# Optimization experiments

Hardware: AMD Instinct MI355X
Metric: run time of the kernel (lower is better)

Reference implementation:

```python
import jax, jax.numpy as jnp
import numpy as np

B, S, T = 128, 2048, 128


def setup_inputs() -> dict:
    key = jax.random.key(0)
    k1, k2, k3, k4, k5, k6 = jax.random.split(key, 6)
    logit = jax.random.normal(k1, (B, S, T), jnp.float32)
    target = jax.random.randint(k2, (B, S), 0, T, dtype=jnp.int32)
    seq_lens = jax.random.randint(k3, (B,), 1, S + 1, dtype=jnp.int32)
    transitions = 0.1 * jax.random.normal(k4, (T, T), jnp.float32)
    start_transitions = 0.1 * jax.random.normal(k5, (T,), jnp.float32)
    end_transitions = 0.1 * jax.random.normal(k6, (T,), jnp.float32)
    return dict(logit=logit, target=target, seq_lens=seq_lens,
                transitions=transitions, start_transitions=start_transitions,
                end_transitions=end_transitions)


def reference(logit, target, seq_lens, transitions, start_transitions, end_transitions):
    # logit: [B,S,T] batch-first; CRF works time-first like the torch code's transpose(0,1)
    em = jnp.transpose(logit, (1, 0, 2))          # [S,B,T]
    tg = target.T                                  # [S,B]
    mask = jnp.arange(S)[:, None] < seq_lens[None, :]  # [S,B]

    # ---- loss: -mean log-likelihood (CRF forward algorithm) ----
    emit = jnp.take_along_axis(em, tg[..., None], -1)[..., 0]   # [S,B]
    trans_sc = transitions[tg[:-1], tg[1:]]                      # [S-1,B]
    num = start_transitions[tg[0]] + emit[0]
    num = num + jnp.sum(jnp.where(mask[1:], emit[1:] + trans_sc, 0.0), axis=0)
    last_tags = jnp.take_along_axis(tg, (seq_lens - 1)[None, :], 0)[0]  # [B]
    num = num + end_transitions[last_tags]

    def fstep(alpha, xs):
        e_t, m_t = xs  # [B,T], [B]
        nxt = jax.nn.logsumexp(alpha[:, :, None] + transitions[None] + e_t[:, None, :], axis=1)
        return jnp.where(m_t[:, None], nxt, alpha), None

    alpha0 = start_transitions[None, :] + em[0]   # [B,T]
    alpha, _ = jax.lax.scan(fstep, alpha0, (em[1:], mask[1:]))
    logZ = jax.nn.logsumexp(alpha + end_transitions[None, :], axis=-1)  # [B]
    loss = -(num - logZ).mean()

    # ---- Viterbi decode ----
    tag_ids = jnp.arange(T, dtype=jnp.int32)

    def vstep(score, xs):
        e_t, m_t = xs
        mat = score[:, :, None] + transitions[None] + e_t[:, None, :]  # [B,Tprev,Tcur]
        best = mat.max(axis=1)
        idx = mat.argmax(axis=1).astype(jnp.int32)
        score = jnp.where(m_t[:, None], best, score)
        idx = jnp.where(m_t[:, None], idx, tag_ids[None, :])  # identity beyond seq end
        return score, idx

    vscore, hist = jax.lax.scan(vstep, alpha0, (em[1:], mask[1:]))  # hist: [S-1,B,T]
    last_tag = jnp.argmax(vscore + end_transitions[None, :], axis=-1).astype(jnp.int32)

    def bstep(tag, idx_t):
        prev = jnp.take_along_axis(idx_t, tag[:, None], 1)[:, 0]
        return prev, prev

    _, tags_prev = jax.lax.scan(bstep, last_tag, hist, reverse=True)  # [S-1,B]
    pred = jnp.concatenate([tags_prev, last_tag[None, :]], axis=0).T  # [B,S]

    # ---- _rearrange_output: swap decoded-tag logit with the max logit ----
    maxidx = jnp.argmax(logit, axis=-1)                         # [B,S]
    maxval = jnp.max(logit, axis=-1)                            # [B,S]
    vval = jnp.take_along_axis(logit, pred[..., None], -1)[..., 0]  # [B,S]
    oh_v = pred[..., None] == tag_ids[None, None, :]
    oh_m = maxidx[..., None] == tag_ids[None, None, :]
    swapped = jnp.where(oh_v, maxval[..., None],
                        jnp.where(oh_m, vval[..., None], logit))
    log_probs = jax.nn.log_softmax(swapped, axis=-1)            # [B,S,T]

    return loss, pred, log_probs
```

## Files before the change

### kernel.cpp

```cpp
#include <hip/hip_runtime.h>
#include <stdint.h>

#define BB 128
#define SS 2048
#define TT 128
#define NSEG 32
#define SEGK 64

#define TRP 129
#define VSTRIDE 136
#define H1OFF 68

typedef float f32x4 __attribute__((ext_vector_type(4)));

#define BAR() asm volatile("s_waitcnt lgkmcnt(0)\n\ts_barrier" ::: "memory")
#define PIN(x) asm volatile("" : "+v"(x))

__device__ __forceinline__ float dpp_swap1_f(float x) {
    int i = __float_as_int(x);
    i = __builtin_amdgcn_update_dpp(0, i, 0xB1, 0xF, 0xF, true);
    return __int_as_float(i);
}
__device__ __forceinline__ int dpp_swap1_i(int x) {
    return __builtin_amdgcn_update_dpp(0, x, 0xB1, 0xF, 0xF, true);
}

#define CLAMPROW(k) (((k) < L) ? (k) : (L - 1))

#define VSTEP(tt, CURP, EREG)                                                 \
{                                                                             \
    const int cur_ = (CURP), nxt_ = 1 - cur_;                                 \
    const float e_ = EREG;                                                    \
    EREG = logit[lbase + (size_t)CLAMPROW((tt) + 4) * TT + j];                \
    const f32x4* sq_ = (const f32x4*)(vecLDS + cur_ * VSTRIDE + h * H1OFF);   \
    float cm_[8];                                                             \
    _Pragma("unroll")                                                         \
    for (int c = 0; c < 8; ++c) {                                             \
        f32x4 pa = sq_[2 * c] + tC[2 * c];                                    \
        f32x4 pb = sq_[2 * c + 1] + tC[2 * c + 1];                            \
        float m01 = fmaxf(pa.x, pa.y), m23 = fmaxf(pa.z, pa.w);               \
        float m45 = fmaxf(pb.x, pb.y), m67 = fmaxf(pb.z, pb.w);               \
        cm_[c] = fmaxf(fmaxf(m01, m23), fmaxf(m45, m67));                     \
    }                                                                         \
    float M_ = fmaxf(fmaxf(fmaxf(cm_[0], cm_[1]), fmaxf(cm_[2], cm_[3])),     \
                     fmaxf(fmaxf(cm_[4], cm_[5]), fmaxf(cm_[6], cm_[7])));    \
    const float Mall_ = fmaxf(M_, dpp_swap1_f(M_));                           \
    const float v_ = Mall_ + e_;               \
    int cwin_ = -1;                                                           \
    _Pragma("unroll")                                                         \
    for (int c = 7; c >= 0; --c) cwin_ = ((cm_[c] + e_) == v_) ? c : cwin_;   \
    int idx_ = 0x7fffffff;                                                    \
    if (cwin_ >= 0) {                                                         \
        const int basei_ = ibase0 + cwin_ * 8;                                \
        const float* tr_ = transLDS + (size_t)basei_ * TRP + j;               \
        const f32x4* sr_ = (const f32x4*)(vecLDS + cur_ * VSTRIDE + h * H1OFF + cwin_ * 8); \
        f32x4 ra_ = sr_[0], rb_ = sr_[1];                                     \
        float q0 = (ra_.x + tr_[0 * TRP]) + e_;                               \
        float q1 = (ra_.y + tr_[1 * TRP]) + e_;                               \
        float q2 = (ra_.z + tr_[2 * TRP]) + e_;                               \
        float q3 = (ra_.w + tr_[3 * TRP]) + e_;                               \
        float q4 = (rb_.x + tr_[4 * TRP]) + e_;                               \
        float q5 = (rb_.y + tr_[5 * TRP]) + e_;                               \
        float q6 = (rb_.z + tr_[6 * TRP]) + e_;                               \
        float q7 = (rb_.w + tr_[7 * TRP]) + e_;                               \
        idx_ = (q7 == v_) ? basei_ + 7 : idx_;                                \
        idx_ = (q6 == v_) ? basei_ + 6 : idx_;                                \
        idx_ = (q5 == v_) ? basei_ + 5 : idx_;                                \
        idx_ = (q4 == v_) ? basei_ + 4 : idx_;                                \
        idx_ = (q3 == v_) ? basei_ + 3 : idx_;                                \
        idx_ = (q2 == v_) ? basei_ + 2 : idx_;                                \
        idx_ = (q1 == v_) ? basei_ + 1 : idx_;                                \
        idx_ = (q0 == v_) ? basei_ + 0 : idx_;                                \
    }                                                                         \
    const int oidx_ = dpp_swap1_i(idx_);                                      \
    idx_ = (oidx_ < idx_) ? oidx_ : idx_;      \
    if (h == 0) {                                                             \
        vecLDS[nxt_ * VSTRIDE + joff] = v_;                                   \
        hb[(size_t)(tt) * TT + j] = (uint8_t)idx_;                            \
    }                                                                         \
    BAR();                                                                    \
}

#define FSTEP(tt, CURP, EREG)                                                 \
{                                                                             \
    const int cur_ = (CURP), nxt_ = 1 - cur_;                                 \
    const float Rcons_ = ringLDS[((tt) - 3) & 3];                             \
    const float Rpub_  = ringLDS[((tt) - 2) & 3];                             \
    const float e_ = EREG;                                                    \
    EREG = logit[lbase + (size_t)CLAMPROW((tt) + 4) * TT + j];                \
    const f32x4* aq_ = (const f32x4*)(vecLDS + cur_ * VSTRIDE + h * H1OFF);   \
    f32x4 s4_ = {0.f, 0.f, 0.f, 0.f}, s4b_ = {0.f, 0.f, 0.f, 0.f};            \
    _Pragma("unroll")                                                         \
    for (int c = 0; c < 16; c += 2) {                                         \
        s4_  = aq_[c] * tE[c] + s4_;                                          \
        s4b_ = aq_[c + 1] * tE[c + 1] + s4b_;                                 \
    }                                                                         \
    f32x4 st_ = s4_ + s4b_;                                                   \
    float Ssum_ = (st_.x + st_.y) + (st_.z + st_.w);                          \
    Ssum_ += dpp_swap1_f(Ssum_);                                              \
    alpha = e_ + Rcons_ + __logf(Ssum_);                                      \
    const float p_ = __expf(alpha - Rpub_);                                   \
    if (h == 0) vecLDS[nxt_ * VSTRIDE + joff] = p_;                           \
    if (tid == 0) ringLDS[(tt) & 3] = alpha;                                  \
    BAR();                                                                    \
}

__attribute__((amdgpu_flat_work_group_size(256, 256)))
__attribute__((amdgpu_waves_per_eu(1, 1)))
__global__ void crf_mainX(const float* __restrict__ logit,
                          const int* __restrict__ seq_lens,
                          const float* __restrict__ trans,
                          const float* __restrict__ startT,
                          const float* __restrict__ endT,
                          const int* __restrict__ target,
                          uint8_t* __restrict__ histG,
                          float* __restrict__ scr_logZ,
                          int* __restrict__ scr_last,
                          float* __restrict__ scr_num)
{
    extern __shared__ float smem[];
    float* transLDS = smem;
    float* vecLDS   = smem + 16512;
    float* ringLDS  = smem + 16512 + 272;
    float* redLDS   = smem + 16512 + 276;
    int*   redILDS  = (int*)(smem + 16512 + 284);
    float* sumLDS   = smem + 16512 + 288;

    const int bid = blockIdx.x;
    const int role = bid >> 7;
    const int b = bid & (BB - 1);
    const int tid = threadIdx.x;
    const int j = tid >> 1;
    const int h = tid & 1;
    const int ibase0 = h << 6;
    const int joff = j + ((j >= 64) ? (H1OFF - 64) : 0);
    const int L = seq_lens[b];
    const size_t lbase = (size_t)b * (SS * TT);

    for (int m = tid; m < TT * TT; m += 256)
        transLDS[(m >> 7) * TRP + (m & 127)] = trans[m];
    __syncthreads();

    float e_a = logit[lbase + (size_t)CLAMPROW(1) * TT + j];
    float e_b = logit[lbase + (size_t)CLAMPROW(2) * TT + j];
    float e_c = logit[lbase + (size_t)CLAMPROW(3) * TT + j];
    float e_d = logit[lbase + (size_t)CLAMPROW(4) * TT + j];

    if (role == 0) {
        f32x4 tC[16];
#pragma unroll
        for (int c = 0; c < 16; ++c) {
            tC[c].x = transLDS[(ibase0 + c * 4 + 0) * TRP + j];
            tC[c].y = transLDS[(ibase0 + c * 4 + 1) * TRP + j];
            tC[c].z = transLDS[(ibase0 + c * 4 + 2) * TRP + j];
            tC[c].w = transLDS[(ibase0 + c * 4 + 3) * TRP + j];
            PIN(tC[c]);
        }
        const float a0 = startT[j] + logit[lbase + j];
        if (h == 0) vecLDS[joff] = a0;
        __syncthreads();

        uint8_t* hb = histG + (size_t)b * (SS * TT);

        int t = 1;
        for (; t + 3 < L; t += 4) {
            VSTEP(t + 0, 0, e_a);
            VSTEP(t + 1, 1, e_b);
            VSTEP(t + 2, 0, e_c);
            VSTEP(t + 3, 1, e_d);
        }
        for (; t < L; ++t) {
            VSTEP(t, ((t - 1) & 1), e_a);
            e_a = e_b; e_b = e_c; e_c = e_d;
        }

        const int fin = (L - 1) & 1;
        if (tid < 128) {
            const int toff = tid + ((tid >= 64) ? (H1OFF - 64) : 0);
            float lv = vecLDS[fin * VSTRIDE + toff] + endT[tid];
            int li = tid;
#pragma unroll
            for (int off = 1; off < 64; off <<= 1) {
                float ov = __shfl_xor(lv, off);
                int oi = __shfl_xor(li, off);
                if (ov > lv || (ov == lv && oi < li)) { lv = ov; li = oi; }
            }
            if ((tid & 63) == 0) { redLDS[tid >> 6] = lv; redILDS[tid >> 6] = li; }
        }
        __syncthreads();
        if (tid == 0) {
            int lt = (redLDS[1] > redLDS[0] ||
                      (redLDS[1] == redLDS[0] && redILDS[1] < redILDS[0]))
                     ? redILDS[1] : redILDS[0];
            scr_last[b] = lt;
        }
        const int colq = (tid & 7) * 16;
        const uint32_t w0 = 0x03020100u + 0x01010101u * (uint32_t)colq;
        const uint4 pat = make_uint4(w0, w0 + 0x04040404u, w0 + 0x08080808u, w0 + 0x0C0C0C0Cu);
        for (int t0 = L; t0 < SS; t0 += 32) {
            int tt = t0 + (tid >> 3);
            if (tt < SS) *(uint4*)(hb + (size_t)tt * TT + colq) = pat;
        }
    } else {
        f32x4 tE[16];
#pragma unroll
        for (int c = 0; c < 16; ++c) {
            tE[c].x = __expf(transLDS[(ibase0 + c * 4 + 0) * TRP + j]);
            tE[c].y = __expf(transLDS[(ibase0 + c * 4 + 1) * TRP + j]);
            tE[c].z = __expf(transLDS[(ibase0 + c * 4 + 2) * TRP + j]);
            tE[c].w = __expf(transLDS[(ibase0 + c * 4 + 3) * TRP + j]);
            PIN(tE[c]);
        }
        const float a0 = startT[j] + logit[lbase + j];
        const float R0 = startT[0] + logit[lbase + 0];
        float alpha = a0;
        if (h == 0) vecLDS[joff] = __expf(a0 - R0);
        if (tid < 4) ringLDS[tid] = R0;
        __syncthreads();

        int t = 1;
        for (; t + 3 < L; t += 4) {
            FSTEP(t + 0, 0, e_a);
            FSTEP(t + 1, 1, e_b);
            FSTEP(t + 2, 0, e_c);
            FSTEP(t + 3, 1, e_d);
        }
        for (; t < L; ++t) {
            FSTEP(t, ((t - 1) & 1), e_a);
            e_a = e_b; e_b = e_c; e_c = e_d;
        }

        const float fval = alpha + endT[j];
        float tmx = fval;
#pragma unroll
        for (int off = 1; off < 64; off <<= 1) tmx = fmaxf(tmx, __shfl_xor(tmx, off));
        if ((tid & 63) == 0) redLDS[4 + (tid >> 6)] = tmx;
        __syncthreads();
        const float gm = fmaxf(fmaxf(redLDS[4], redLDS[5]), fmaxf(redLDS[6], redLDS[7]));
        float se = (h == 0) ? __expf(fval - gm) : 0.f;
#pragma unroll
        for (int off = 1; off < 64; off <<= 1) se += __shfl_xor(se, off);
        if ((tid & 63) == 0) sumLDS[tid >> 6] = se;
        __syncthreads();
        if (tid == 0)
            scr_logZ[b] = gm + __logf(sumLDS[0] + sumLDS[1] + sumLDS[2] + sumLDS[3]);
        __syncthreads();

        float acc = 0.f;
        for (int tt = tid; tt < L; tt += 256) {
            int tg = target[b * SS + tt];
            acc += logit[((size_t)b * SS + tt) * TT + tg];
            if (tt >= 1) acc += trans[target[b * SS + tt - 1] * TT + tg];
        }
#pragma unroll
        for (int off = 1; off < 64; off <<= 1) acc += __shfl_xor(acc, off);
        if ((tid & 63) == 0) sumLDS[tid >> 6] = acc;
        __syncthreads();
        if (tid == 0) {
            float tot = sumLDS[0] + sumLDS[1] + sumLDS[2] + sumLDS[3];
            tot += startT[target[b * SS]] + endT[target[b * SS + L - 1]];
            scr_num[b] = tot;
        }
    }
}

__global__ void crf_btseg(uint8_t* __restrict__ histG)
{
    const int c = blockIdx.x;
    const int b = blockIdx.y;
    const int tid = threadIdx.x;
    __shared__ __align__(16) uint8_t hl[SEGK * TT];

    const int lo = (c == 0) ? 1 : c * SEGK;
    const int nr = (c == 0) ? 63 : 64;
    const uint8_t* src = histG + (size_t)b * (SS * TT) + (size_t)lo * TT;
    for (int k = tid; k < (nr * TT) / 16; k += 128)
        ((uint4*)hl)[k] = ((const uint4*)src)[k];
    __syncthreads();

    int tau = tid;
    uint32_t w[16];
#pragma unroll
    for (int q = 0; q < 16; ++q) w[q] = 0u;
    if (c == 0) {
#pragma unroll
        for (int r = 62; r >= 0; --r) {
            tau = hl[r * TT + tau];
            w[r >> 2] |= ((uint32_t)tau) << ((r & 3) * 8);
        }
    } else {
#pragma unroll
        for (int r = 63; r >= 0; --r) {
            tau = hl[r * TT + tau];
            w[r >> 2] |= ((uint32_t)tau) << ((r & 3) * 8);
        }
    }
    uint4* dst = (uint4*)(histG + (size_t)b * (SS * TT) + (size_t)c * 8192 + (size_t)tid * 64);
    dst[0] = make_uint4(w[0], w[1], w[2], w[3]);
    dst[1] = make_uint4(w[4], w[5], w[6], w[7]);
    dst[2] = make_uint4(w[8], w[9], w[10], w[11]);
    dst[3] = make_uint4(w[12], w[13], w[14], w[15]);
}

__global__ void crf_btchain(const uint8_t* __restrict__ histG,
                            const int* __restrict__ scr_last,
                            int* __restrict__ scr_bt,
                            float* __restrict__ out_pred)
{
    const int b = threadIdx.x;
    if (b >= BB) return;
    int tau = scr_last[b];
    out_pred[(size_t)b * SS + (SS - 1)] = (float)tau;
    for (int c = NSEG - 1; c >= 0; --c) {
        scr_bt[b * NSEG + c] = tau;
        tau = histG[(size_t)b * (SS * TT) + (size_t)c * 8192 + (size_t)tau * 64];
    }
}

__global__ void crf_btfill(const uint8_t* __restrict__ histG,
                           const int* __restrict__ scr_bt,
                           float* __restrict__ out_pred)
{
    const int c = blockIdx.x;
    const int b = blockIdx.y;
    const int s = threadIdx.x;
    if (c == 0 && s > 62) return;
    const int js = scr_bt[b * NSEG + c];
    uint8_t v = histG[(size_t)b * (SS * TT) + (size_t)c * 8192 + (size_t)js * 64 + s];
    const int pos = (c == 0) ? s : (c * SEGK - 1 + s);
    out_pred[(size_t)b * SS + pos] = (float)v;
}

__global__ void crf_loss(const float* __restrict__ scr_logZ, const float* __restrict__ scr_num,
                         float* __restrict__ out)
{
    const int tid = threadIdx.x;
    __shared__ float p2[2];
    float v = (tid < BB) ? (scr_logZ[tid] - scr_num[tid]) : 0.0f;
#pragma unroll
    for (int off = 1; off < 64; off <<= 1) v += __shfl_xor(v, off);
    if ((tid & 63) == 0) p2[tid >> 6] = v;
    __syncthreads();
    if (tid == 0) out[0] = (p2[0] + p2[1]) / (float)BB;
}

__global__ void crf_logprobs(const float* __restrict__ logit,
                             const float* __restrict__ predF,
                             float* __restrict__ outLP)
{
    const int wid = threadIdx.x >> 6;
    const int lane = threadIdx.x & 63;
    const size_t row = (size_t)blockIdx.x * 4 + wid;
    const float2* rp = (const float2*)(logit + row * TT);
    float2 v = rp[lane];
    const int pred = (int)predF[row];

    float mv; int mi;
    if (v.y > v.x) { mv = v.y; mi = lane * 2 + 1; }
    else           { mv = v.x; mi = lane * 2; }
#pragma unroll
    for (int off = 1; off < 64; off <<= 1) {
        float ov = __shfl_xor(mv, off);
        int oi = __shfl_xor(mi, off);
        if (ov > mv || (ov == mv && oi < mi)) { mv = ov; mi = oi; }
    }
    float se = __expf(v.x - mv) + __expf(v.y - mv);
#pragma unroll
    for (int off = 1; off < 64; off <<= 1) se += __shfl_xor(se, off);
    const float lse = __logf(se);

    float px = __shfl(v.x, pred >> 1);
    float py = __shfl(v.y, pred >> 1);
    float vp = (pred & 1) ? py : px;

    float ox = (lane * 2 == pred) ? mv : ((lane * 2 == mi) ? vp : v.x);
    float oy = (lane * 2 + 1 == pred) ? mv : ((lane * 2 + 1 == mi) ? vp : v.y);
    float* op = outLP + row * TT + lane * 2;
    op[0] = (ox - mv) - lse;
    op[1] = (oy - mv) - lse;
}

extern "C" void kernel_launch(void* const* d_in, const int* in_sizes, int n_in,
                              void* d_out, int out_size, void* d_ws, size_t ws_size,
                              hipStream_t stream)
{
    const float* logit    = (const float*)d_in[0];
    const int*   target   = (const int*)d_in[1];
    const int*   seq_lens = (const int*)d_in[2];
    const float* trans    = (const float*)d_in[3];
    const float* startT   = (const float*)d_in[4];
    const float* endT     = (const float*)d_in[5];

    float* out      = (float*)d_out;
    float* out_pred = out + 1;
    float* outLP    = out + 1 + (size_t)BB * SS;
    uint8_t* histG  = (uint8_t*)(out + 262148);
    float* scr      = out + ((size_t)1 + (size_t)BB * SS + (size_t)BB * SS * TT - 4480);
    float* scr_logZ = scr;
    float* scr_num  = scr + 128;
    int*   scr_last = (int*)(scr + 256);
    int*   scr_bt   = (int*)(scr + 384);

    const int dynLDS = (16512 + 292) * 4;
    hipFuncSetAttribute((const void*)crf_mainX,
                        hipFuncAttributeMaxDynamicSharedMemorySize, dynLDS);

    crf_mainX<<<2 * BB, 256, dynLDS, stream>>>(logit, seq_lens, trans, startT, endT,
                                               target, histG, scr_logZ, scr_last, scr_num);
    crf_btseg<<<dim3(NSEG, BB), 128, 0, stream>>>(histG);
    crf_btchain<<<1, 128, 0, stream>>>(histG, scr_last, scr_bt, out_pred);
    crf_btfill<<<dim3(NSEG, BB), 64, 0, stream>>>(histG, scr_bt, out_pred);
    crf_loss<<<1, 128, 0, stream>>>(scr_logZ, scr_num, out);
    crf_logprobs<<<(BB * SS) / 4, 256, 0, stream>>>(logit, out_pred, outLP);
}
```

Baseline: 1.506 ms.

## Stage emissions in double-buffered LDS chunks and batch Viterbi history stores

Replaces the per-step scalar global loads of emission values (four-step register prefetch) with chunked vectorized loads of 32 timesteps into registers, then stored to a double-buffered LDS region while the previous chunk is consumed. Viterbi backpointers are written to an LDS staging buffer and flushed to global memory once per chunk with 16-byte stores instead of byte stores every step. The aim is to take global memory latency and narrow stores off the serial recurrence's critical path. The cost is more LDS, an extra barrier per chunk, and 16 live vector registers holding the prefetched chunk across the step loop.

```diff
diff --git a/kernel.cpp b/kernel.cpp
--- a/kernel.cpp
+++ b/kernel.cpp
@@ -6,6 +6,7 @@
 #define TT 128
 #define NSEG 32
 #define SEGK 64
+#define CHK 32
 
 #define TRP 129
 #define VSTRIDE 136
@@ -25,13 +26,10 @@
     return __builtin_amdgcn_update_dpp(0, x, 0xB1, 0xF, 0xF, true);
 }
 
-#define CLAMPROW(k) (((k) < L) ? (k) : (L - 1))
-
-#define VSTEP(tt, CURP, EREG)                                                 \
+#define VSTEP(slot, CURP)                                                     \
 {                                                                             \
     const int cur_ = (CURP), nxt_ = 1 - cur_;                                 \
-    const float e_ = EREG;                                                    \
-    EREG = logit[lbase + (size_t)CLAMPROW((tt) + 4) * TT + j];                \
+    const float e_ = ecur[(slot) * TT + j];                                   \
     const f32x4* sq_ = (const f32x4*)(vecLDS + cur_ * VSTRIDE + h * H1OFF);   \
     float cm_[8];                                                             \
     _Pragma("unroll")                                                         \
@@ -76,18 +74,18 @@
     idx_ = (oidx_ < idx_) ? oidx_ : idx_;      \
     if (h == 0) {                                                             \
         vecLDS[nxt_ * VSTRIDE + joff] = v_;                                   \
-        hb[(size_t)(tt) * TT + j] = (uint8_t)idx_;                            \
+        hsLDS[(slot) * TT + j] = (uint8_t)idx_;                               \
     }                                                                         \
     BAR();                                                                    \
 }
 
-#define FSTEP(tt, CURP, EREG)                                                 \
+#define FSTEP(slot, CURP)                                                     \
 {                                                                             \
     const int cur_ = (CURP), nxt_ = 1 - cur_;                                 \
-    const float Rcons_ = ringLDS[((tt) - 3) & 3];                             \
-    const float Rpub_  = ringLDS[((tt) - 2) & 3];                             \
-    const float e_ = EREG;                                                    \
-    EREG = logit[lbase + (size_t)CLAMPROW((tt) + 4) * TT + j];                \
+    const int tt_ = tc + (slot);                                              \
+    const float Rcons_ = ringLDS[(tt_ - 3) & 3];                              \
+    const float Rpub_  = ringLDS[(tt_ - 2) & 3];                              \
+    const float e_ = ecur[(slot) * TT + j];                                   \
     const f32x4* aq_ = (const f32x4*)(vecLDS + cur_ * VSTRIDE + h * H1OFF);   \
     f32x4 s4_ = {0.f, 0.f, 0.f, 0.f}, s4b_ = {0.f, 0.f, 0.f, 0.f};            \
     _Pragma("unroll")                                                         \
@@ -101,8 +99,26 @@
     alpha = e_ + Rcons_ + __logf(Ssum_);                                      \
     const float p_ = __expf(alpha - Rpub_);                                   \
     if (h == 0) vecLDS[nxt_ * VSTRIDE + joff] = p_;                           \
-    if (tid == 0) ringLDS[(tt) & 3] = alpha;                                  \
+    if (tid == 0) ringLDS[tt_ & 3] = alpha;                                   \
     BAR();                                                                    \
+}
+
+#define ECHUNK_LOAD(s0)                                                       \
+{                                                                             \
+    _Pragma("unroll")                                                         \
+    for (int p = 0; p < 4; ++p) {                                             \
+        int f = p * 1024 + tid * 4;                                           \
+        int gf = (s0) * TT + f;                                               \
+        int mx = (SS - 1) * TT + (f & (TT - 1));                              \
+        gf = (gf < mx) ? gf : mx;                                             \
+        ec[p] = *(const f32x4*)(logit + lbase + gf);                          \
+    }                                                                         \
+}
+#define ECHUNK_STORE(dstbuf)                                                  \
+{                                                                             \
+    _Pragma("unroll")                                                         \
+    for (int p = 0; p < 4; ++p)                                               \
+        *(f32x4*)((dstbuf) + p * 1024 + tid * 4) = ec[p];                     \
 }
 
 __attribute__((amdgpu_flat_work_group_size(256, 256)))
@@ -125,6 +141,8 @@
     float* redLDS   = smem + 16512 + 276;
     int*   redILDS  = (int*)(smem + 16512 + 284);
     float* sumLDS   = smem + 16512 + 288;
+    float* eLDS     = smem + 16804;
+    uint8_t* hsLDS  = (uint8_t*)(smem + 16804 + 8192);
 
     const int bid = blockIdx.x;
     const int role = bid >> 7;
@@ -137,14 +155,14 @@
     const int L = seq_lens[b];
     const size_t lbase = (size_t)b * (SS * TT);
 
+    f32x4 ec[4];
+
+    ECHUNK_LOAD(1);
+    ECHUNK_STORE(eLDS);
+
     for (int m = tid; m < TT * TT; m += 256)
         transLDS[(m >> 7) * TRP + (m & 127)] = trans[m];
     __syncthreads();
-
-    float e_a = logit[lbase + (size_t)CLAMPROW(1) * TT + j];
-    float e_b = logit[lbase + (size_t)CLAMPROW(2) * TT + j];
-    float e_c = logit[lbase + (size_t)CLAMPROW(3) * TT + j];
-    float e_d = logit[lbase + (size_t)CLAMPROW(4) * TT + j];
 
     if (role == 0) {
         f32x4 tC[16];
@@ -162,16 +180,26 @@
 
         uint8_t* hb = histG + (size_t)b * (SS * TT);
 
-        int t = 1;
-        for (; t + 3 < L; t += 4) {
-            VSTEP(t + 0, 0, e_a);
-            VSTEP(t + 1, 1, e_b);
-            VSTEP(t + 2, 0, e_c);
-            VSTEP(t + 3, 1, e_d);
-        }
-        for (; t < L; ++t) {
-            VSTEP(t, ((t - 1) & 1), e_a);
-            e_a = e_b; e_b = e_c; e_c = e_d;
+        int c = 0;
+        for (int tc = 1; tc < L; tc += CHK, ++c) {
+            const int tend = (tc + CHK < L) ? tc + CHK : L;
+            const int n = tend - tc;
+            const float* ecur = eLDS + (c & 1) * (CHK * TT);
+            const bool more = (tc + CHK) < L;
+            if (more) ECHUNK_LOAD(tc + CHK);
+
+            for (int s = 0; s + 1 < n; s += 2) { VSTEP(s, 0); VSTEP(s + 1, 1); }
+            if (n & 1) { VSTEP(n - 1, 0); }
+
+            {
+                const int lr = tid >> 3, cq = (tid & 7) * 16;
+                if (lr < n) {
+                    uint4 v = *(const uint4*)(hsLDS + lr * TT + cq);
+                    *(uint4*)(hb + (size_t)(tc + lr) * TT + cq) = v;
+                }
+            }
+            if (more) ECHUNK_STORE(eLDS + ((c + 1) & 1) * (CHK * TT));
+            BAR();
         }
 
         const int fin = (L - 1) & 1;
@@ -218,16 +246,19 @@
         if (tid < 4) ringLDS[tid] = R0;
         __syncthreads();
 
-        int t = 1;
-        for (; t + 3 < L; t += 4) {
-            FSTEP(t + 0, 0, e_a);
-            FSTEP(t + 1, 1, e_b);
-            FSTEP(t + 2, 0, e_c);
-            FSTEP(t + 3, 1, e_d);
-        }
-        for (; t < L; ++t) {
-            FSTEP(t, ((t - 1) & 1), e_a);
-            e_a = e_b; e_b = e_c; e_c = e_d;
+        int c = 0;
+        for (int tc = 1; tc < L; tc += CHK, ++c) {
+            const int tend = (tc + CHK < L) ? tc + CHK : L;
+            const int n = tend - tc;
+            const float* ecur = eLDS + (c & 1) * (CHK * TT);
+            const bool more = (tc + CHK) < L;
+            if (more) ECHUNK_LOAD(tc + CHK);
+
+            for (int s = 0; s + 1 < n; s += 2) { FSTEP(s, 0); FSTEP(s + 1, 1); }
+            if (n & 1) { FSTEP(n - 1, 0); }
+
+            if (more) ECHUNK_STORE(eLDS + ((c + 1) & 1) * (CHK * TT));
+            BAR();
         }
 
         const float fval = alpha + endT[j];
@@ -401,7 +432,7 @@
     int*   scr_last = (int*)(scr + 256);
     int*   scr_bt   = (int*)(scr + 384);
 
-    const int dynLDS = (16512 + 292) * 4;
+    const int dynLDS = (16804 + 2 * CHK * TT + (CHK * TT) / 4) * 4;
     hipFuncSetAttribute((const void*)crf_mainX,
                         hipFuncAttributeMaxDynamicSharedMemorySize, dynLDS);
 
```

New measurement: 1.529 ms. Within noise of the previous version (+1.5%).
